# Kernel tuning notes

Measured on AMD Instinct MI355X. Metric: run time of the kernel, lower is better.

Reference implementation:

```python
import jax, jax.numpy as jnp
import numpy as np

T_STEPS = 100
T_EMB = 16
EPS = 1e-8


def sin_emb(t, dim):
    # sinusoidal_time_embedding: [cos(t*f), sin(t*f)] with f = exp(-log(1e4)*i/half)
    half = dim // 2
    freqs = jnp.exp(-jnp.log(jnp.float32(10000.0)) * jnp.arange(half, dtype=jnp.float32) / half)
    a = t.astype(jnp.float32)[:, None] * freqs[None, :]
    return jnp.concatenate([jnp.cos(a), jnp.sin(a)], axis=-1)


def lstm_layer(x_tbf, W_ih, W_hh, b):
    # x_tbf: [T, B, F]; torch gate order i, f, g, o
    B = x_tbf.shape[1]
    H = W_hh.shape[1]

    def step(carry, x_t):
        h, c = carry
        g = x_t @ W_ih.T + h @ W_hh.T + b
        i, f, gg, o = jnp.split(g, 4, axis=-1)
        c = jax.nn.sigmoid(f) * c + jax.nn.sigmoid(i) * jnp.tanh(gg)
        h = jax.nn.sigmoid(o) * jnp.tanh(c)
        return (h, c), h

    z = jnp.zeros((B, H), x_tbf.dtype)
    (h, c), ys = jax.lax.scan(step, (z, z), x_tbf)
    return ys, h


def _forward(x_hist, x_future, y0, turb_idx, pred_steps, init_noise, turb_emb,
             W_ih0, W_hh0, b_ih0, b_hh0, W_ih1, W_hh1, b_ih1, b_hh1,
             W1, b1, W2, b2, W3, b3):
    betas = jnp.linspace(1e-4, 0.02, T_STEPS).astype(jnp.float32)
    alphas = 1.0 - betas
    alpha_bars = jnp.cumprod(alphas)

    B = x_hist.shape[0]
    emb = turb_emb[turb_idx]  # [B, E]
    eh = jnp.broadcast_to(emb[:, None, :], (B, x_hist.shape[1], emb.shape[1]))
    ef = jnp.broadcast_to(emb[:, None, :], (B, x_future.shape[1], emb.shape[1]))
    xh = jnp.concatenate([x_hist, eh], axis=-1).transpose(1, 0, 2)    # [T_in, B, F+E]
    xf = jnp.concatenate([x_future, ef], axis=-1).transpose(1, 0, 2)  # [P, B, exo+E]

    ys0, _ = lstm_layer(xh, W_ih0, W_hh0, b_ih0 + b_hh0)
    _, enc_out = lstm_layer(ys0, W_ih1, W_hh1, b_ih1 + b_hh1)         # [B, H] = h[-1]

    def mlp(x):
        h = jax.nn.relu(x @ W1.T + b1)
        h = jax.nn.relu(h @ W2.T + b2)
        return h @ W3.T + b3

    def ar_step(prev_y, xs):
        exo_t, step, y_init = xs
        cond = jnp.concatenate([enc_out, exo_t, prev_y], axis=1)  # [B, cond_dim]
        h_e = sin_emb(jnp.full((B,), step), T_EMB)

        def dstep(y, t):
            t_e = sin_emb(jnp.full((B,), t), T_EMB)
            eps_hat = mlp(jnp.concatenate([cond, y, t_e, h_e], axis=1))  # [B,1]
            b_t, a_t, ab_t = betas[t], alphas[t], alpha_bars[t]
            pred_x0 = (y - jnp.sqrt(1.0 - ab_t) * eps_hat) / (jnp.sqrt(ab_t) + EPS)
            mean = (y - b_t / (jnp.sqrt(1.0 - ab_t) + EPS) * eps_hat) / (jnp.sqrt(a_t) + EPS)
            # eval mode -> deterministic sampling: posterior noise term is zero
            return jnp.where(t == 0, pred_x0, mean), None

        y, _ = jax.lax.scan(dstep, y_init, jnp.arange(T_STEPS - 1, -1, -1))
        return y, y[:, 0]

    _, seq = jax.lax.scan(ar_step, y0, (xf, jnp.arange(pred_steps), init_noise))
    return seq.T[:, :, None]  # [B, pred_steps, 1]


def setup_inputs() -> dict:
    key = jax.random.key(0)
    ks = list(jax.random.split(key, 24))
    kit = iter(ks)
    B, T_IN, F_IN, EXO, EMB, PRED, HID, NTURB = 1024, 96, 8, 6, 16, 8, 128, 100
    in0 = F_IN + EMB                 # 24
    cond_dim = HID + EXO + EMB + 1   # 151
    in_mlp = cond_dim + 1 + T_EMB + T_EMB  # 184

    def nrm(shape, s=0.05):
        return jax.random.normal(next(kit), shape, jnp.float32) * s

    return {
        'x_hist': jax.random.normal(next(kit), (B, T_IN, F_IN), jnp.float32),
        'x_future': jax.random.normal(next(kit), (B, PRED, EXO), jnp.float32),
        'y0': jnp.zeros((B, 1), jnp.float32),
        'turb_idx': jax.random.randint(next(kit), (B,), 0, NTURB),
        'pred_steps': PRED,
        'init_noise': jax.random.normal(next(kit), (PRED, B, 1), jnp.float32),
        'turb_emb': nrm((NTURB, EMB), 0.1),
        'W_ih0': nrm((4 * HID, in0)), 'W_hh0': nrm((4 * HID, HID)),
        'b_ih0': jnp.zeros((4 * HID,), jnp.float32), 'b_hh0': jnp.zeros((4 * HID,), jnp.float32),
        'W_ih1': nrm((4 * HID, HID)), 'W_hh1': nrm((4 * HID, HID)),
        'b_ih1': jnp.zeros((4 * HID,), jnp.float32), 'b_hh1': jnp.zeros((4 * HID,), jnp.float32),
        'W1': nrm((HID, in_mlp)), 'b1': jnp.zeros((HID,), jnp.float32),
        'W2': nrm((HID, HID)), 'b2': jnp.zeros((HID,), jnp.float32),
        'W3': nrm((1, HID)), 'b3': jnp.zeros((1,), jnp.float32),
    }


def reference(x_hist, x_future, y0, turb_idx, pred_steps, init_noise, turb_emb,
              W_ih0, W_hh0, b_ih0, b_hh0, W_ih1, W_hh1, b_ih1, b_hh1,
              W1, b1, W2, b2, W3, b3):
    return _forward(x_hist, x_future, y0, turb_idx, pred_steps, init_noise, turb_emb,
                    W_ih0, W_hh0, b_ih0, b_hh0, W_ih1, W_hh1, b_ih1, b_hh1,
                    W1, b1, W2, b2, W3, b3)
```

## Files before the change

### kernel.cpp

```cpp
#include <hip/hip_runtime.h>
#include <hip/hip_fp16.h>
#include <stdint.h>


typedef __attribute__((ext_vector_type(2))) _Float16 half2_t;
typedef __attribute__((ext_vector_type(8))) _Float16 v8h;
typedef __attribute__((ext_vector_type(4))) float v4f;

#define DEV __device__ __forceinline__

DEV uint32_t pack2f(float a, float b) {
  __half ha = __float2half_rn(a), hb = __float2half_rn(b);
  return (uint32_t)__half_as_ushort(ha) | ((uint32_t)__half_as_ushort(hb) << 16);
}

DEV float2 up2(uint32_t u) {
  half2_t h = __builtin_bit_cast(half2_t, u);
  return make_float2((float)h.x, (float)h.y);
}

DEV float fast_ex2(float x) {
#if __has_builtin(__builtin_amdgcn_exp2f)
  return __builtin_amdgcn_exp2f(x);
#else
  return exp2f(x);
#endif
}
DEV float fast_rcp(float x) {
#if __has_builtin(__builtin_amdgcn_rcpf)
  return __builtin_amdgcn_rcpf(x);
#else
  return 1.f / x;
#endif
}
DEV float sigm(float x) { return fast_rcp(1.f + fast_ex2(-1.4426950408889634f * x)); }
DEV float tanh_f(float x) {
  return 2.f * fast_rcp(1.f + fast_ex2(-2.8853900817779268f * x)) - 1.f;
}

DEV uint32_t pk_add(uint32_t a, uint32_t b) {
  return __builtin_bit_cast(uint32_t,
      __builtin_bit_cast(half2_t, a) + __builtin_bit_cast(half2_t, b));
}

DEV uint32_t pk_relufma(uint32_t w, uint32_t y, uint32_t b) {
  half2_t r = __builtin_bit_cast(half2_t, w) * __builtin_bit_cast(half2_t, y) +
              __builtin_bit_cast(half2_t, b);
  half2_t z = {(_Float16)0.f, (_Float16)0.f};
#if __has_builtin(__builtin_elementwise_max)
  r = __builtin_elementwise_max(r, z);
#else
  uint32_t u = __builtin_bit_cast(uint32_t, r);
  uint32_t mask = ((u >> 15) & 1u) * 0xFFFFu | ((u >> 31) & 1u) * 0xFFFF0000u;
  r = __builtin_bit_cast(half2_t, u & ~mask);
#endif
  return __builtin_bit_cast(uint32_t, r);
}

DEV uint32_t pk_max0(uint32_t a) {
  half2_t z = {(_Float16)0.f, (_Float16)0.f};
#if __has_builtin(__builtin_elementwise_max)
  return __builtin_bit_cast(uint32_t,
      __builtin_elementwise_max(__builtin_bit_cast(half2_t, a), z));
#else
  uint32_t mask = ((a >> 15) & 1u) * 0xFFFFu | ((a >> 31) & 1u) * 0xFFFF0000u;
  return a & ~mask;
#endif
}

DEV uint32_t cvtpk(float y) {
#if __has_builtin(__builtin_amdgcn_cvt_pkrtz)
  return __builtin_bit_cast(uint32_t, __builtin_amdgcn_cvt_pkrtz(y, y));
#else
  return pack2f(y, y);
#endif
}

DEV uint32_t cvtpk2(float a, float b) {
#if __has_builtin(__builtin_amdgcn_cvt_pkrtz)
  return __builtin_bit_cast(uint32_t, __builtin_amdgcn_cvt_pkrtz(a, b));
#else
  return pack2f(a, b);
#endif
}

DEV half2_t pk_fma2(uint32_t a, uint32_t b, half2_t c) {
  return __builtin_bit_cast(half2_t, a) * __builtin_bit_cast(half2_t, b) + c;
}

static constexpr size_t OFF_XH  = 0;
static constexpr size_t OFF_W0  = 4718592;
static constexpr size_t OFF_BS0 = 4882432;
static constexpr size_t OFF_W1L = 4884480;
static constexpr size_t OFF_BS1 = 5146624;
static constexpr size_t OFF_W2P = 5148672;
static constexpr size_t OFF_ENC = 5181440;
static constexpr size_t OFF_YS0 = 5705728;
static constexpr size_t OFF_TPJ = 30871552;
static constexpr size_t OFF_HPJ = 30897152;
static constexpr size_t OFF_CC  = 30899200;

__global__ void k_prep_xh(const float* __restrict__ xh, const int* __restrict__ tix,
                          const float* __restrict__ temb, uint32_t* __restrict__ out) {
  int idx = blockIdx.x * 256 + threadIdx.x;
  if (idx >= 96 * 1024 * 12) return;
  int m = idx % 12;
  int tb = idx / 12;
  int b = tb & 1023, t = tb >> 10;
  int k0 = 2 * m, k1 = k0 + 1;
  float v0 = (k0 < 8) ? xh[(b * 96 + t) * 8 + k0] : temb[tix[b] * 16 + (k0 - 8)];
  float v1 = (k1 < 8) ? xh[(b * 96 + t) * 8 + k1] : temb[tix[b] * 16 + (k1 - 8)];
  out[idx] = pack2f(v0, v1);
}

__global__ void k_prep_w(const float* __restrict__ Wih0, const float* __restrict__ Whh0,
                         const float* __restrict__ bih0, const float* __restrict__ bhh0,
                         const float* __restrict__ Wih1, const float* __restrict__ Whh1,
                         const float* __restrict__ bih1, const float* __restrict__ bhh1,
                         const float* __restrict__ W2, const float* __restrict__ W1,
                         uint32_t* __restrict__ w0p, uint32_t* __restrict__ w1p,
                         uint32_t* __restrict__ w2p, float* __restrict__ bs0,
                         float* __restrict__ bs1, uint32_t* __restrict__ tpj,
                         uint32_t* __restrict__ hpj, float2* __restrict__ ccg) {
  int idx = blockIdx.x * 256 + threadIdx.x;
  if (idx < 40960) {
    int w = idx / 5120;
    int r = idx % 5120;
    int T = r / 1280; r %= 1280;
    int f = r / 256;  r %= 256;
    int l = r >> 2, c = r & 3;
    int m = l & 15, qf = l >> 4;
    int g = (m & 3) * 128 + w * 16 + (m >> 2) * 4 + T;
    int k0 = f * 32 + qf * 8 + 2 * c, k1 = k0 + 1;
    float a = (k0 < 24) ? Wih0[g * 24 + k0] : ((k0 < 152) ? Whh0[g * 128 + k0 - 24] : 0.f);
    float b = (k1 < 24) ? Wih0[g * 24 + k1] : ((k1 < 152) ? Whh0[g * 128 + k1 - 24] : 0.f);
    w0p[idx] = pack2f(a, b);
  } else if (idx < 106496) {
    int i = idx - 40960;
    int w = i / 8192;
    int r = i % 8192;
    int T = r / 2048; r %= 2048;
    int f = r / 256;  r %= 256;
    int l = r >> 2, c = r & 3;
    int m = l & 15, qf = l >> 4;
    int g = (m & 3) * 128 + w * 16 + (m >> 2) * 4 + T;
    int k0 = f * 32 + qf * 8 + 2 * c, k1 = k0 + 1;
    float a = (k0 < 128) ? Wih1[g * 128 + k0] : Whh1[g * 128 + k0 - 128];
    float b = (k1 < 128) ? Wih1[g * 128 + k1] : Whh1[g * 128 + k1 - 128];
    w1p[i] = pack2f(a, b);
  } else if (idx < 114688) {
    int i = idx - 106496;
    w2p[i] = pack2f(W2[2 * i], W2[2 * i + 1]);
  } else if (idx < 115200) {
    int i = idx - 114688;
    bs0[i] = bih0[i] + bhh0[i];
  } else if (idx < 115712) {
    int i = idx - 115200;
    bs1[i] = bih1[i] + bhh1[i];
  } else if (idx < 122112) {
    int i = idx - 115712;
    int t = i / 64;
    int r = i % 64;
    int q = r / 16, pi = r % 16;
    int k0 = (pi >> 2) * 32 + q * 8 + (pi & 3) * 2;
    float te[16];
#pragma unroll
    for (int j = 0; j < 8; j++) {
      float f = expf(-logf(10000.f) * (float)j / 8.f);
      float a = (float)t * f;
      te[j] = cosf(a);
      te[j + 8] = sinf(a);
    }
    float s0 = 0.f, s1 = 0.f;
#pragma unroll
    for (int j = 0; j < 16; j++) {
      s0 += W1[k0 * 184 + 152 + j] * te[j];
      s1 += W1[(k0 + 1) * 184 + 152 + j] * te[j];
    }
    tpj[i] = pack2f((float)__half2float(__float2half_rn(s0)),
                    (float)__half2float(__float2half_rn(s1)));
  } else if (idx < 122624) {
    int i = idx - 122112;
    int s = i / 64;
    int kp = i % 64;
    float te[16];
#pragma unroll
    for (int j = 0; j < 8; j++) {
      float f = expf(-logf(10000.f) * (float)j / 8.f);
      float a = (float)s * f;
      te[j] = cosf(a);
      te[j + 8] = sinf(a);
    }
    float s0 = 0.f, s1 = 0.f;
#pragma unroll
    for (int j = 0; j < 16; j++) {
      s0 += W1[(2 * kp) * 184 + 168 + j] * te[j];
      s1 += W1[(2 * kp + 1) * 184 + 168 + j] * te[j];
    }
    hpj[i] = pack2f((float)__half2float(__float2half_rn(s0)),
                    (float)__half2float(__float2half_rn(s1)));
  } else if (idx < 122724) {
    int qq = idx - 122624;
    float ab = 1.f, beta = 0.f;
    for (int i = 0; i <= qq; i++) {
      beta = 1e-4f + (0.02f - 1e-4f) * (float)i / 99.f;
      ab *= (1.f - beta);
    }
    float cs, cd;
    if (qq == 0) { cs = sqrtf(1.f - ab); cd = 1.f / (sqrtf(ab) + 1e-8f); }
    else { cs = beta / (sqrtf(1.f - ab) + 1e-8f); cd = 1.f / (sqrtf(1.f - beta) + 1e-8f); }
    ccg[qq] = make_float2(cs * cd, cd);
  }
}

__global__ __launch_bounds__(512, 2) void k_lstm0(const uint32_t* __restrict__ xh16,
                                                  const uint32_t* __restrict__ w0A,
                                                  const float* __restrict__ bs0,
                                                  __half* __restrict__ ys0) {
  __shared__ __align__(16) __half inb[2][16][160];
  const int tid = threadIdx.x;
  const int w = tid >> 6, l = tid & 63;
  const int n = l & 15, ql = l >> 4;
  const int ju = w * 16 + ql * 4;
  const int bbase = blockIdx.x * 16;

  uint4 Af[4][5];
#pragma unroll
  for (int T = 0; T < 4; T++)
#pragma unroll
    for (int f = 0; f < 5; f++)
      Af[T][f] = ((const uint4*)w0A)[((w * 4 + T) * 5 + f) * 64 + l];
  float bias[4][4];
#pragma unroll
  for (int T = 0; T < 4; T++)
#pragma unroll
    for (int r = 0; r < 4; r++) bias[T][r] = bs0[r * 128 + ju + T];

  for (int i = tid; i < 2560; i += 512) ((uint32_t*)inb)[i] = 0u;
  __syncthreads();
  if (tid < 192) {
    int b = tid / 12, m = tid % 12;
    ((uint32_t*)&inb[0][b][0])[m] = xh16[(0 * 1024 + bbase + b) * 12 + m];
  }
  float cst[4] = {0.f, 0.f, 0.f, 0.f};
  __syncthreads();

  for (int t = 0; t < 96; t++) {
    const int cur = t & 1, nxt = cur ^ 1;
    uint32_t sx = 0;
    int sb = 0, sm = 0;
    if (t < 95 && tid < 192) {
      sb = tid / 12; sm = tid % 12;
      sx = xh16[((t + 1) * 1024 + bbase + sb) * 12 + sm];
    }
    v4f acc[4];
#pragma unroll
    for (int T = 0; T < 4; T++) acc[T] = (v4f){0.f, 0.f, 0.f, 0.f};
#pragma unroll
    for (int f = 0; f < 5; f++) {
      uint4 bu = *(const uint4*)&inb[cur][n][f * 32 + ql * 8];
      v8h Bv = __builtin_bit_cast(v8h, bu);
#pragma unroll
      for (int T = 0; T < 4; T++)
        acc[T] = __builtin_amdgcn_mfma_f32_16x16x32_f16(
            __builtin_bit_cast(v8h, Af[T][f]), Bv, acc[T], 0, 0, 0);
    }
    float hv[4];
#pragma unroll
    for (int T = 0; T < 4; T++) {
      float gi = acc[T][0] + bias[T][0];
      float gf = acc[T][1] + bias[T][1];
      float gg = acc[T][2] + bias[T][2];
      float go = acc[T][3] + bias[T][3];
      float c = sigm(gf) * cst[T] + sigm(gi) * tanh_f(gg);
      cst[T] = c;
      hv[T] = sigm(go) * tanh_f(c);
    }
    uint32_t h01 = pack2f(hv[0], hv[1]), h23 = pack2f(hv[2], hv[3]);
    *(uint2*)&inb[nxt][n][24 + ju] = make_uint2(h01, h23);
    *(uint2*)((__half*)ys0 + (size_t)(t * 1024 + bbase + n) * 128 + ju) = make_uint2(h01, h23);
    if (t < 95 && tid < 192) ((uint32_t*)&inb[nxt][sb][0])[sm] = sx;
    __syncthreads();
  }
}

__global__ __launch_bounds__(512, 2) void k_lstm1(const uint32_t* __restrict__ ys0u,
                                                  const uint32_t* __restrict__ w1A,
                                                  const float* __restrict__ bs1,
                                                  float* __restrict__ enc) {
  __shared__ __align__(16) __half inb[2][16][264];
  const int tid = threadIdx.x;
  const int w = tid >> 6, l = tid & 63;
  const int n = l & 15, ql = l >> 4;
  const int ju = w * 16 + ql * 4;
  const int bbase = blockIdx.x * 16;
  const int sb = tid >> 5, sc = tid & 31;

  uint4 Af[4][8];
#pragma unroll
  for (int T = 0; T < 4; T++)
#pragma unroll
    for (int f = 0; f < 8; f++)
      Af[T][f] = ((const uint4*)w1A)[((w * 4 + T) * 8 + f) * 64 + l];
  float bias[4][4];
#pragma unroll
  for (int T = 0; T < 4; T++)
#pragma unroll
    for (int r = 0; r < 4; r++) bias[T][r] = bs1[r * 128 + ju + T];

  for (int i = tid; i < 4224; i += 512) ((uint32_t*)inb)[i] = 0u;
  __syncthreads();
  {
    uint2 v = ((const uint2*)ys0u)[(size_t)(0 * 1024 + bbase + sb) * 32 + sc];
    *(uint2*)&inb[0][sb][sc * 4] = v;
  }
  float cst[4] = {0.f, 0.f, 0.f, 0.f};
  __syncthreads();

  for (int t = 0; t < 96; t++) {
    const int cur = t & 1, nxt = cur ^ 1;
    uint2 sv = make_uint2(0u, 0u);
    if (t < 95)
      sv = ((const uint2*)ys0u)[(size_t)((t + 1) * 1024 + bbase + sb) * 32 + sc];
    v4f acc[4];
#pragma unroll
    for (int T = 0; T < 4; T++) acc[T] = (v4f){0.f, 0.f, 0.f, 0.f};
#pragma unroll
    for (int f = 0; f < 8; f++) {
      uint4 bu = *(const uint4*)&inb[cur][n][f * 32 + ql * 8];
      v8h Bv = __builtin_bit_cast(v8h, bu);
#pragma unroll
      for (int T = 0; T < 4; T++)
        acc[T] = __builtin_amdgcn_mfma_f32_16x16x32_f16(
            __builtin_bit_cast(v8h, Af[T][f]), Bv, acc[T], 0, 0, 0);
    }
    float hv[4];
#pragma unroll
    for (int T = 0; T < 4; T++) {
      float gi = acc[T][0] + bias[T][0];
      float gf = acc[T][1] + bias[T][1];
      float gg = acc[T][2] + bias[T][2];
      float go = acc[T][3] + bias[T][3];
      float c = sigm(gf) * cst[T] + sigm(gi) * tanh_f(gg);
      cst[T] = c;
      hv[T] = sigm(go) * tanh_f(c);
    }
    *(uint2*)&inb[nxt][n][128 + ju] = make_uint2(pack2f(hv[0], hv[1]), pack2f(hv[2], hv[3]));
    if (t < 95) *(uint2*)&inb[nxt][sb][sc * 4] = sv;
    if (t == 95)
      *(float4*)&enc[(size_t)(bbase + n) * 128 + ju] = make_float4(hv[0], hv[1], hv[2], hv[3]);
    __syncthreads();
  }
}

__global__ __launch_bounds__(256, 1) void k_diff(
    const float* __restrict__ xfut, const float* __restrict__ y0,
    const int* __restrict__ tix, const float* __restrict__ noise,
    const float* __restrict__ temb, const float* __restrict__ W1,
    const float* __restrict__ b1, const float* __restrict__ b2,
    const float* __restrict__ W3, const float* __restrict__ b3,
    const uint32_t* __restrict__ w2p, const float* __restrict__ enc,
    const uint32_t* __restrict__ tpj, const uint32_t* __restrict__ hpj,
    const float2* __restrict__ ccG, float* __restrict__ out) {
  __shared__ uint32_t W1sL[128 * 65];
  __shared__ uint32_t W1xL[128 * 29];
  __shared__ uint32_t encPL[16 * 65];
  __shared__ uint32_t embPL[16 * 9];
  __shared__ uint32_t encdL[256 * 17];
  __shared__ __align__(16) float partL[2][16][20];

  const int tid = threadIdx.x;
  const int w = tid >> 6, l = tid & 63;
  const int m = l & 15, q = l >> 4;
  const int gbase = blockIdx.x * 16;
  const uint4* tpj4 = (const uint4*)tpj;

  for (int i = tid; i < 128 * 64; i += 256) {
    int r = i >> 6, c = i & 63;
    W1sL[r * 65 + c] = pack2f(W1[r * 184 + 2 * c], W1[r * 184 + 2 * c + 1]);
  }
  for (int i = tid; i < 128 * 28; i += 256) {
    int r = i / 28, c = i % 28;
    W1xL[r * 29 + c] = pack2f(W1[r * 184 + 128 + 2 * c], W1[r * 184 + 129 + 2 * c]);
  }
  for (int i = tid; i < 16 * 64; i += 256) {
    int bq = i >> 6, c = i & 63;
    encPL[bq * 65 + c] = pack2f(enc[(gbase + bq) * 128 + 2 * c],
                                enc[(gbase + bq) * 128 + 2 * c + 1]);
  }
  for (int i = tid; i < 16 * 8; i += 256) {
    int bq = i >> 3, c = i & 7;
    const float* er = temb + tix[gbase + bq] * 16;
    embPL[bq * 9 + c] = pack2f(er[2 * c], er[2 * c + 1]);
  }
  __syncthreads();

  for (int pi = 0; pi < 16; pi++) {
    int k0 = (pi >> 2) * 32 + q * 8 + (pi & 3) * 2;
    half2_t a0 = {(_Float16)0.f, (_Float16)0.f};
    half2_t a1 = a0;
    const uint32_t* wr0 = &W1sL[k0 * 65];
    const uint32_t* wr1 = &W1sL[(k0 + 1) * 65];
    const uint32_t* ep = &encPL[m * 65];
#pragma unroll 8
    for (int c = 0; c < 64; c++) {
      half2_t e = __builtin_bit_cast(half2_t, ep[c]);
      a0 += __builtin_bit_cast(half2_t, wr0[c]) * e;
      a1 += __builtin_bit_cast(half2_t, wr1[c]) * e;
    }
#pragma unroll
    for (int c = 0; c < 8; c++) {
      half2_t e = __builtin_bit_cast(half2_t, embPL[m * 9 + c]);
      a0 += __builtin_bit_cast(half2_t, W1xL[k0 * 29 + 3 + c]) * e;
      a1 += __builtin_bit_cast(half2_t, W1xL[(k0 + 1) * 29 + 3 + c]) * e;
    }
    float e0 = b1[k0] + (float)a0.x + (float)a0.y;
    float e1 = b1[k0 + 1] + (float)a1.x + (float)a1.y;
    encdL[tid * 17 + pi] = pack2f(e0, e1);
  }

  uint4 Bf[2][4];
  {
    const uint4* w2u4 = (const uint4*)w2p;
#pragma unroll
    for (int j = 0; j < 2; j++)
#pragma unroll
      for (int f = 0; f < 4; f++)
        Bf[j][f] = w2u4[((2 * w + j) * 16 + m) * 16 + f * 4 + q];
  }
  uint32_t b2P[4], w3P[4];
#pragma unroll
  for (int j = 0; j < 2; j++) {
    int tt = 2 * w + j;
    b2P[2 * j]     = pack2f(b2[tt * 16 + q * 4 + 0], b2[tt * 16 + q * 4 + 1]);
    b2P[2 * j + 1] = pack2f(b2[tt * 16 + q * 4 + 2], b2[tt * 16 + q * 4 + 3]);
    w3P[2 * j]     = pack2f(W3[tt * 16 + q * 4 + 0], W3[tt * 16 + q * 4 + 1]);
    w3P[2 * j + 1] = pack2f(W3[tt * 16 + q * 4 + 2], W3[tt * 16 + q * 4 + 3]);
  }
  const float b3v = b3[0];
  const int pslot = w * 4 + q;

  uint32_t w1yP[16];
#pragma unroll
  for (int pi = 0; pi < 16; pi++) {
    int k0 = (pi >> 2) * 32 + q * 8 + (pi & 3) * 2;
    uint32_t ua = W1xL[k0 * 29 + 11];
    uint32_t ub = W1xL[(k0 + 1) * 29 + 11];
    w1yP[pi] = (ua >> 16) | (ub & 0xFFFF0000u);
  }

  float prev_y = y0[gbase + m];
  __syncthreads();

  float y = 0.f;
  float2 ccv = make_float2(0.f, 0.f);
  uint32_t bph[16], bt[16];
  const v4f zf = (v4f){0.f, 0.f, 0.f, 0.f};

#define DSTEP(t_, PB)                                                          \
  do {                                                                         \
    const int tn_ = ((t_) > 0) ? (t_) - 1 : 0;                                 \
    const uint4* tg_ = tpj4 + (size_t)(tn_ * 4 + q) * 4;    \
    uint4 t0 = tg_[0], t1 = tg_[1], t2 = tg_[2], t3 = tg_[3];                  \
    float2 cck_ = ccG[tn_];                                                    \
    const uint32_t yP = cvtpk(y);                                              \
    uint4 au[4];                                                               \
    _Pragma("unroll")                                                          \
    for (int f = 0; f < 4; f++) {                                              \
      au[f].x = pk_relufma(w1yP[4 * f + 0], yP, bt[4 * f + 0]);                \
      au[f].y = pk_relufma(w1yP[4 * f + 1], yP, bt[4 * f + 1]);                \
      au[f].z = pk_relufma(w1yP[4 * f + 2], yP, bt[4 * f + 2]);                \
      au[f].w = pk_relufma(w1yP[4 * f + 3], yP, bt[4 * f + 3]);                \
    }                                                                          \
                             \
    v4f a0 = __builtin_amdgcn_mfma_f32_16x16x32_f16(                           \
        __builtin_bit_cast(v8h, Bf[0][0]), __builtin_bit_cast(v8h, au[0]), zf, 0, 0, 0); \
    v4f b0 = __builtin_amdgcn_mfma_f32_16x16x32_f16(                           \
        __builtin_bit_cast(v8h, Bf[0][1]), __builtin_bit_cast(v8h, au[1]), zf, 0, 0, 0); \
    v4f a1 = __builtin_amdgcn_mfma_f32_16x16x32_f16(                           \
        __builtin_bit_cast(v8h, Bf[1][0]), __builtin_bit_cast(v8h, au[0]), zf, 0, 0, 0); \
    v4f b1x = __builtin_amdgcn_mfma_f32_16x16x32_f16(                          \
        __builtin_bit_cast(v8h, Bf[1][1]), __builtin_bit_cast(v8h, au[1]), zf, 0, 0, 0); \
    a0 = __builtin_amdgcn_mfma_f32_16x16x32_f16(                               \
        __builtin_bit_cast(v8h, Bf[0][2]), __builtin_bit_cast(v8h, au[2]), a0, 0, 0, 0); \
    b0 = __builtin_amdgcn_mfma_f32_16x16x32_f16(                               \
        __builtin_bit_cast(v8h, Bf[0][3]), __builtin_bit_cast(v8h, au[3]), b0, 0, 0, 0); \
    a1 = __builtin_amdgcn_mfma_f32_16x16x32_f16(                               \
        __builtin_bit_cast(v8h, Bf[1][2]), __builtin_bit_cast(v8h, au[2]), a1, 0, 0, 0); \
    b1x = __builtin_amdgcn_mfma_f32_16x16x32_f16(                              \
        __builtin_bit_cast(v8h, Bf[1][3]), __builtin_bit_cast(v8h, au[3]), b1x, 0, 0, 0); \
    v4f c0 = a0 + b0, c1 = a1 + b1x;                                           \
                      \
    half2_t runA = {(_Float16)0.f, (_Float16)0.f};                             \
    half2_t runB = runA;                                                       \
    {                                                                          \
      uint32_t h01 = pk_max0(pk_add(cvtpk2(c0[0], c0[1]), b2P[0]));            \
      uint32_t h23 = pk_max0(pk_add(cvtpk2(c0[2], c0[3]), b2P[1]));            \
      runA = pk_fma2(h01, w3P[0], runA);                                       \
      runA = pk_fma2(h23, w3P[1], runA);                                       \
      uint32_t g01 = pk_max0(pk_add(cvtpk2(c1[0], c1[1]), b2P[2]));            \
      uint32_t g23 = pk_max0(pk_add(cvtpk2(c1[2], c1[3]), b2P[3]));            \
      runB = pk_fma2(g01, w3P[2], runB);                                       \
      runB = pk_fma2(g23, w3P[3], runB);                                       \
    }                                                                          \
    partL[PB][m][pslot] = ((float)runA.x + (float)runA.y) +                    \
                          ((float)runB.x + (float)runB.y);                     \
    const float pre_ = ccv.y * y - ccv.x * b3v;           \
    __syncthreads();                                                           \
               \
    const v4f* pl_ = (const v4f*)&partL[PB][m][0];                             \
    v4f p0_ = pl_[0], p1_ = pl_[1], p2_ = pl_[2], p3_ = pl_[3];                \
    bt[0] = pk_add(bph[0], t0.x);   bt[1] = pk_add(bph[1], t0.y);              \
    bt[2] = pk_add(bph[2], t0.z);   bt[3] = pk_add(bph[3], t0.w);              \
    bt[4] = pk_add(bph[4], t1.x);   bt[5] = pk_add(bph[5], t1.y);              \
    bt[6] = pk_add(bph[6], t1.z);   bt[7] = pk_add(bph[7], t1.w);              \
    bt[8] = pk_add(bph[8], t2.x);   bt[9] = pk_add(bph[9], t2.y);              \
    bt[10] = pk_add(bph[10], t2.z); bt[11] = pk_add(bph[11], t2.w);            \
    bt[12] = pk_add(bph[12], t3.x); bt[13] = pk_add(bph[13], t3.y);            \
    bt[14] = pk_add(bph[14], t3.z); bt[15] = pk_add(bph[15], t3.w);            \
    v4f ps_ = (p0_ + p1_) + (p2_ + p3_);                                       \
    y = pre_ - ccv.x * ((ps_[0] + ps_[1]) + (ps_[2] + ps_[3]));                \
    ccv = cck_;                                                                \
  } while (0)

  for (int s = 0; s < 8; s++) {
    float yn = noise[s * 1024 + gbase + m];
    float xf[6];
#pragma unroll
    for (int i = 0; i < 6; i++) xf[i] = xfut[((gbase + m) * 8 + s) * 6 + i];
#pragma unroll
    for (int pi = 0; pi < 16; pi++) {
      int k0 = (pi >> 2) * 32 + q * 8 + (pi & 3) * 2;
      float2 ed = up2(encdL[tid * 17 + pi]);
      float e0 = ed.x, e1 = ed.y;
#pragma unroll
      for (int c = 0; c < 3; c++) {
        float2 w0v = up2(W1xL[k0 * 29 + c]);
        float2 w1v = up2(W1xL[(k0 + 1) * 29 + c]);
        e0 += w0v.x * xf[2 * c] + w0v.y * xf[2 * c + 1];
        e1 += w1v.x * xf[2 * c] + w1v.y * xf[2 * c + 1];
      }
      e0 += up2(W1xL[k0 * 29 + 11]).x * prev_y;
      e1 += up2(W1xL[(k0 + 1) * 29 + 11]).x * prev_y;
      float2 hh = up2(hpj[s * 64 + (k0 >> 1)]);
      e0 += hh.x;
      e1 += hh.y;
      bph[pi] = pack2f(e0, e1);
    }

    y = yn;
    {
      const uint4* tg = tpj4 + (size_t)(99 * 4 + q) * 4;
      uint4 t0 = tg[0], t1 = tg[1], t2 = tg[2], t3 = tg[3];
      bt[0] = pk_add(bph[0], t0.x);   bt[1] = pk_add(bph[1], t0.y);
      bt[2] = pk_add(bph[2], t0.z);   bt[3] = pk_add(bph[3], t0.w);
      bt[4] = pk_add(bph[4], t1.x);   bt[5] = pk_add(bph[5], t1.y);
      bt[6] = pk_add(bph[6], t1.z);   bt[7] = pk_add(bph[7], t1.w);
      bt[8] = pk_add(bph[8], t2.x);   bt[9] = pk_add(bph[9], t2.y);
      bt[10] = pk_add(bph[10], t2.z); bt[11] = pk_add(bph[11], t2.w);
      bt[12] = pk_add(bph[12], t3.x); bt[13] = pk_add(bph[13], t3.y);
      bt[14] = pk_add(bph[14], t3.z); bt[15] = pk_add(bph[15], t3.w);
    }
    ccv = ccG[99];

    for (int it = 0; it < 50; it++) {
      DSTEP(99 - 2 * it, 0);
      DSTEP(98 - 2 * it, 1);
    }

    if (w == 0 && l < 16) out[(gbase + l) * 8 + s] = y;
    prev_y = y;
  }
#undef DSTEP
}

extern "C" void kernel_launch(void* const* d_in, const int* in_sizes, int n_in,
                              void* d_out, int out_size, void* d_ws, size_t ws_size,
                              hipStream_t stream) {
  const float* x_hist    = (const float*)d_in[0];
  const float* x_future  = (const float*)d_in[1];
  const float* y0        = (const float*)d_in[2];
  const int*   turb_idx  = (const int*)d_in[3];
  const float* init_noise = (const float*)d_in[5];
  const float* turb_emb  = (const float*)d_in[6];
  const float* W_ih0     = (const float*)d_in[7];
  const float* W_hh0     = (const float*)d_in[8];
  const float* b_ih0     = (const float*)d_in[9];
  const float* b_hh0     = (const float*)d_in[10];
  const float* W_ih1     = (const float*)d_in[11];
  const float* W_hh1     = (const float*)d_in[12];
  const float* b_ih1     = (const float*)d_in[13];
  const float* b_hh1     = (const float*)d_in[14];
  const float* W1        = (const float*)d_in[15];
  const float* b1        = (const float*)d_in[16];
  const float* W2        = (const float*)d_in[17];
  const float* b2        = (const float*)d_in[18];
  const float* W3        = (const float*)d_in[19];
  const float* b3        = (const float*)d_in[20];

  char* ws = (char*)d_ws;
  uint32_t* xh16 = (uint32_t*)(ws + OFF_XH);
  uint32_t* w0p  = (uint32_t*)(ws + OFF_W0);
  float*    bs0  = (float*)(ws + OFF_BS0);
  uint32_t* w1p  = (uint32_t*)(ws + OFF_W1L);
  float*    bs1  = (float*)(ws + OFF_BS1);
  uint32_t* w2p  = (uint32_t*)(ws + OFF_W2P);
  float*    encf = (float*)(ws + OFF_ENC);
  __half*   ys0h = (__half*)(ws + OFF_YS0);
  uint32_t* tpjw = (uint32_t*)(ws + OFF_TPJ);
  uint32_t* hpjw = (uint32_t*)(ws + OFF_HPJ);
  float2*   ccw  = (float2*)(ws + OFF_CC);

  k_prep_xh<<<4608, 256, 0, stream>>>(x_hist, turb_idx, turb_emb, xh16);
  k_prep_w<<<480, 256, 0, stream>>>(W_ih0, W_hh0, b_ih0, b_hh0,
                                    W_ih1, W_hh1, b_ih1, b_hh1,
                                    W2, W1, w0p, w1p, w2p, bs0, bs1,
                                    tpjw, hpjw, ccw);
  k_lstm0<<<64, 512, 0, stream>>>(xh16, w0p, bs0, ys0h);
  k_lstm1<<<64, 512, 0, stream>>>((const uint32_t*)ys0h, w1p, bs1, encf);
  k_diff<<<64, 256, 0, stream>>>(x_future, y0, turb_idx, init_noise, turb_emb,
                                 W1, b1, b2, W3, b3, w2p, encf,
                                 tpjw, hpjw, ccw, (float*)d_out);
}
```

Baseline: 633.2 us.

## Interleave two independent batch chains per diffusion block to halve barriers

The diffusion kernel now processes 32 batch rows per block as two independent 16-row chains (A and B), so 32 blocks launch instead of 64. Each denoising step computes both chains before one shared barrier, giving the scheduler independent MFMA and ALU work to interleave and spreading the per-step sync cost over twice the rows. In exchange, fewer CUs are used, register pressure roughly doubles for the bias arrays, and shared-memory use grows.

```diff
diff --git a/kernel.cpp b/kernel.cpp
--- a/kernel.cpp
+++ b/kernel.cpp
@@ -364,15 +364,15 @@
     const float2* __restrict__ ccG, float* __restrict__ out) {
   __shared__ uint32_t W1sL[128 * 65];
   __shared__ uint32_t W1xL[128 * 29];
-  __shared__ uint32_t encPL[16 * 65];
-  __shared__ uint32_t embPL[16 * 9];
-  __shared__ uint32_t encdL[256 * 17];
-  __shared__ __align__(16) float partL[2][16][20];
+  __shared__ uint32_t encPL[32 * 65];
+  __shared__ uint32_t embPL[32 * 9];
+  __shared__ uint32_t encdL[2][256 * 17];
+  __shared__ __align__(16) float partL[2][2][16][20];
 
   const int tid = threadIdx.x;
   const int w = tid >> 6, l = tid & 63;
   const int m = l & 15, q = l >> 4;
-  const int gbase = blockIdx.x * 16;
+  const int gbase = blockIdx.x * 32;
   const uint4* tpj4 = (const uint4*)tpj;
 
   for (int i = tid; i < 128 * 64; i += 256) {
@@ -383,40 +383,44 @@
     int r = i / 28, c = i % 28;
     W1xL[r * 29 + c] = pack2f(W1[r * 184 + 128 + 2 * c], W1[r * 184 + 129 + 2 * c]);
   }
-  for (int i = tid; i < 16 * 64; i += 256) {
+  for (int i = tid; i < 32 * 64; i += 256) {
     int bq = i >> 6, c = i & 63;
     encPL[bq * 65 + c] = pack2f(enc[(gbase + bq) * 128 + 2 * c],
                                 enc[(gbase + bq) * 128 + 2 * c + 1]);
   }
-  for (int i = tid; i < 16 * 8; i += 256) {
+  for (int i = tid; i < 32 * 8; i += 256) {
     int bq = i >> 3, c = i & 7;
     const float* er = temb + tix[gbase + bq] * 16;
     embPL[bq * 9 + c] = pack2f(er[2 * c], er[2 * c + 1]);
   }
   __syncthreads();
 
-  for (int pi = 0; pi < 16; pi++) {
-    int k0 = (pi >> 2) * 32 + q * 8 + (pi & 3) * 2;
-    half2_t a0 = {(_Float16)0.f, (_Float16)0.f};
-    half2_t a1 = a0;
-    const uint32_t* wr0 = &W1sL[k0 * 65];
-    const uint32_t* wr1 = &W1sL[(k0 + 1) * 65];
-    const uint32_t* ep = &encPL[m * 65];
+#pragma unroll
+  for (int ch = 0; ch < 2; ch++) {
+    const int bm = ch * 16 + m;
+    for (int pi = 0; pi < 16; pi++) {
+      int k0 = (pi >> 2) * 32 + q * 8 + (pi & 3) * 2;
+      half2_t a0 = {(_Float16)0.f, (_Float16)0.f};
+      half2_t a1 = a0;
+      const uint32_t* wr0 = &W1sL[k0 * 65];
+      const uint32_t* wr1 = &W1sL[(k0 + 1) * 65];
+      const uint32_t* ep = &encPL[bm * 65];
 #pragma unroll 8
-    for (int c = 0; c < 64; c++) {
-      half2_t e = __builtin_bit_cast(half2_t, ep[c]);
-      a0 += __builtin_bit_cast(half2_t, wr0[c]) * e;
-      a1 += __builtin_bit_cast(half2_t, wr1[c]) * e;
-    }
-#pragma unroll
-    for (int c = 0; c < 8; c++) {
-      half2_t e = __builtin_bit_cast(half2_t, embPL[m * 9 + c]);
-      a0 += __builtin_bit_cast(half2_t, W1xL[k0 * 29 + 3 + c]) * e;
-      a1 += __builtin_bit_cast(half2_t, W1xL[(k0 + 1) * 29 + 3 + c]) * e;
-    }
-    float e0 = b1[k0] + (float)a0.x + (float)a0.y;
-    float e1 = b1[k0 + 1] + (float)a1.x + (float)a1.y;
-    encdL[tid * 17 + pi] = pack2f(e0, e1);
+      for (int c = 0; c < 64; c++) {
+        half2_t e = __builtin_bit_cast(half2_t, ep[c]);
+        a0 += __builtin_bit_cast(half2_t, wr0[c]) * e;
+        a1 += __builtin_bit_cast(half2_t, wr1[c]) * e;
+      }
+#pragma unroll
+      for (int c = 0; c < 8; c++) {
+        half2_t e = __builtin_bit_cast(half2_t, embPL[bm * 9 + c]);
+        a0 += __builtin_bit_cast(half2_t, W1xL[k0 * 29 + 3 + c]) * e;
+        a1 += __builtin_bit_cast(half2_t, W1xL[(k0 + 1) * 29 + 3 + c]) * e;
+      }
+      float e0 = b1[k0] + (float)a0.x + (float)a0.y;
+      float e1 = b1[k0 + 1] + (float)a1.x + (float)a1.y;
+      encdL[ch][tid * 17 + pi] = pack2f(e0, e1);
+    }
   }
 
   uint4 Bf[2][4];
@@ -449,30 +453,26 @@
     w1yP[pi] = (ua >> 16) | (ub & 0xFFFF0000u);
   }
 
-  float prev_y = y0[gbase + m];
+  float prevA = y0[gbase + m];
+  float prevB = y0[gbase + 16 + m];
   __syncthreads();
 
-  float y = 0.f;
+  float yA = 0.f, yB = 0.f;
   float2 ccv = make_float2(0.f, 0.f);
-  uint32_t bph[16], bt[16];
+  uint32_t bphA[16], btA[16], bphB[16], btB[16];
   const v4f zf = (v4f){0.f, 0.f, 0.f, 0.f};
 
-#define DSTEP(t_, PB)                                                          \
+#define CHAIN_COMPUTE(Y, BT, CH, PB)                                           \
   do {                                                                         \
-    const int tn_ = ((t_) > 0) ? (t_) - 1 : 0;                                 \
-    const uint4* tg_ = tpj4 + (size_t)(tn_ * 4 + q) * 4;    \
-    uint4 t0 = tg_[0], t1 = tg_[1], t2 = tg_[2], t3 = tg_[3];                  \
-    float2 cck_ = ccG[tn_];                                                    \
-    const uint32_t yP = cvtpk(y);                                              \
+    const uint32_t yP = cvtpk(Y);                                              \
     uint4 au[4];                                                               \
     _Pragma("unroll")                                                          \
     for (int f = 0; f < 4; f++) {                                              \
-      au[f].x = pk_relufma(w1yP[4 * f + 0], yP, bt[4 * f + 0]);                \
-      au[f].y = pk_relufma(w1yP[4 * f + 1], yP, bt[4 * f + 1]);                \
-      au[f].z = pk_relufma(w1yP[4 * f + 2], yP, bt[4 * f + 2]);                \
-      au[f].w = pk_relufma(w1yP[4 * f + 3], yP, bt[4 * f + 3]);                \
+      au[f].x = pk_relufma(w1yP[4 * f + 0], yP, BT[4 * f + 0]);                \
+      au[f].y = pk_relufma(w1yP[4 * f + 1], yP, BT[4 * f + 1]);                \
+      au[f].z = pk_relufma(w1yP[4 * f + 2], yP, BT[4 * f + 2]);                \
+      au[f].w = pk_relufma(w1yP[4 * f + 3], yP, BT[4 * f + 3]);                \
     }                                                                          \
-                             \
     v4f a0 = __builtin_amdgcn_mfma_f32_16x16x32_f16(                           \
         __builtin_bit_cast(v8h, Bf[0][0]), __builtin_bit_cast(v8h, au[0]), zf, 0, 0, 0); \
     v4f b0 = __builtin_amdgcn_mfma_f32_16x16x32_f16(                           \
@@ -490,7 +490,6 @@
     b1x = __builtin_amdgcn_mfma_f32_16x16x32_f16(                              \
         __builtin_bit_cast(v8h, Bf[1][3]), __builtin_bit_cast(v8h, au[3]), b1x, 0, 0, 0); \
     v4f c0 = a0 + b0, c1 = a1 + b1x;                                           \
-                      \
     half2_t runA = {(_Float16)0.f, (_Float16)0.f};                             \
     half2_t runB = runA;                                                       \
     {                                                                          \
@@ -503,63 +502,103 @@
       runB = pk_fma2(g01, w3P[2], runB);                                       \
       runB = pk_fma2(g23, w3P[3], runB);                                       \
     }                                                                          \
-    partL[PB][m][pslot] = ((float)runA.x + (float)runA.y) +                    \
-                          ((float)runB.x + (float)runB.y);                     \
-    const float pre_ = ccv.y * y - ccv.x * b3v;           \
+    partL[PB][CH][m][pslot] = ((float)runA.x + (float)runA.y) +                \
+                              ((float)runB.x + (float)runB.y);                 \
+  } while (0)
+
+#define DSTEP(t_, PB)                                                          \
+  do {                                                                         \
+    const int tn_ = ((t_) > 0) ? (t_) - 1 : 0;                                 \
+    const uint4* tg_ = tpj4 + (size_t)(tn_ * 4 + q) * 4;           \
+    uint4 t0 = tg_[0], t1 = tg_[1], t2 = tg_[2], t3 = tg_[3];                  \
+    float2 cck_ = ccG[tn_];                                                    \
+    CHAIN_COMPUTE(yA, btA, 0, PB);                                             \
+    CHAIN_COMPUTE(yB, btB, 1, PB);                                             \
+    const float preA_ = ccv.y * yA - ccv.x * b3v;                              \
+    const float preB_ = ccv.y * yB - ccv.x * b3v;                              \
     __syncthreads();                                                           \
-               \
-    const v4f* pl_ = (const v4f*)&partL[PB][m][0];                             \
-    v4f p0_ = pl_[0], p1_ = pl_[1], p2_ = pl_[2], p3_ = pl_[3];                \
-    bt[0] = pk_add(bph[0], t0.x);   bt[1] = pk_add(bph[1], t0.y);              \
-    bt[2] = pk_add(bph[2], t0.z);   bt[3] = pk_add(bph[3], t0.w);              \
-    bt[4] = pk_add(bph[4], t1.x);   bt[5] = pk_add(bph[5], t1.y);              \
-    bt[6] = pk_add(bph[6], t1.z);   bt[7] = pk_add(bph[7], t1.w);              \
-    bt[8] = pk_add(bph[8], t2.x);   bt[9] = pk_add(bph[9], t2.y);              \
-    bt[10] = pk_add(bph[10], t2.z); bt[11] = pk_add(bph[11], t2.w);            \
-    bt[12] = pk_add(bph[12], t3.x); bt[13] = pk_add(bph[13], t3.y);            \
-    bt[14] = pk_add(bph[14], t3.z); bt[15] = pk_add(bph[15], t3.w);            \
-    v4f ps_ = (p0_ + p1_) + (p2_ + p3_);                                       \
-    y = pre_ - ccv.x * ((ps_[0] + ps_[1]) + (ps_[2] + ps_[3]));                \
+    const v4f* plA_ = (const v4f*)&partL[PB][0][m][0];                         \
+    v4f pA0_ = plA_[0], pA1_ = plA_[1], pA2_ = plA_[2], pA3_ = plA_[3];        \
+    const v4f* plB_ = (const v4f*)&partL[PB][1][m][0];                         \
+    v4f pB0_ = plB_[0], pB1_ = plB_[1], pB2_ = plB_[2], pB3_ = plB_[3];        \
+    btA[0] = pk_add(bphA[0], t0.x);   btA[1] = pk_add(bphA[1], t0.y);          \
+    btA[2] = pk_add(bphA[2], t0.z);   btA[3] = pk_add(bphA[3], t0.w);          \
+    btA[4] = pk_add(bphA[4], t1.x);   btA[5] = pk_add(bphA[5], t1.y);          \
+    btA[6] = pk_add(bphA[6], t1.z);   btA[7] = pk_add(bphA[7], t1.w);          \
+    btA[8] = pk_add(bphA[8], t2.x);   btA[9] = pk_add(bphA[9], t2.y);          \
+    btA[10] = pk_add(bphA[10], t2.z); btA[11] = pk_add(bphA[11], t2.w);        \
+    btA[12] = pk_add(bphA[12], t3.x); btA[13] = pk_add(bphA[13], t3.y);        \
+    btA[14] = pk_add(bphA[14], t3.z); btA[15] = pk_add(bphA[15], t3.w);        \
+    btB[0] = pk_add(bphB[0], t0.x);   btB[1] = pk_add(bphB[1], t0.y);          \
+    btB[2] = pk_add(bphB[2], t0.z);   btB[3] = pk_add(bphB[3], t0.w);          \
+    btB[4] = pk_add(bphB[4], t1.x);   btB[5] = pk_add(bphB[5], t1.y);          \
+    btB[6] = pk_add(bphB[6], t1.z);   btB[7] = pk_add(bphB[7], t1.w);          \
+    btB[8] = pk_add(bphB[8], t2.x);   btB[9] = pk_add(bphB[9], t2.y);          \
+    btB[10] = pk_add(bphB[10], t2.z); btB[11] = pk_add(bphB[11], t2.w);        \
+    btB[12] = pk_add(bphB[12], t3.x); btB[13] = pk_add(bphB[13], t3.y);        \
+    btB[14] = pk_add(bphB[14], t3.z); btB[15] = pk_add(bphB[15], t3.w);        \
+    v4f psA_ = (pA0_ + pA1_) + (pA2_ + pA3_);                                  \
+    v4f psB_ = (pB0_ + pB1_) + (pB2_ + pB3_);                                  \
+    yA = preA_ - ccv.x * ((psA_[0] + psA_[1]) + (psA_[2] + psA_[3]));          \
+    yB = preB_ - ccv.x * ((psB_[0] + psB_[1]) + (psB_[2] + psB_[3]));          \
     ccv = cck_;                                                                \
   } while (0)
 
   for (int s = 0; s < 8; s++) {
-    float yn = noise[s * 1024 + gbase + m];
-    float xf[6];
-#pragma unroll
-    for (int i = 0; i < 6; i++) xf[i] = xfut[((gbase + m) * 8 + s) * 6 + i];
+    float ynA = noise[s * 1024 + gbase + m];
+    float ynB = noise[s * 1024 + gbase + 16 + m];
+    float xfA[6], xfB[6];
+#pragma unroll
+    for (int i = 0; i < 6; i++) {
+      xfA[i] = xfut[((gbase + m) * 8 + s) * 6 + i];
+      xfB[i] = xfut[((gbase + 16 + m) * 8 + s) * 6 + i];
+    }
 #pragma unroll
     for (int pi = 0; pi < 16; pi++) {
       int k0 = (pi >> 2) * 32 + q * 8 + (pi & 3) * 2;
-      float2 ed = up2(encdL[tid * 17 + pi]);
-      float e0 = ed.x, e1 = ed.y;
+      float2 hh = up2(hpj[s * 64 + (k0 >> 1)]);
+      float2 edA = up2(encdL[0][tid * 17 + pi]);
+      float2 edB = up2(encdL[1][tid * 17 + pi]);
+      float eA0 = edA.x + hh.x, eA1 = edA.y + hh.y;
+      float eB0 = edB.x + hh.x, eB1 = edB.y + hh.y;
 #pragma unroll
       for (int c = 0; c < 3; c++) {
         float2 w0v = up2(W1xL[k0 * 29 + c]);
         float2 w1v = up2(W1xL[(k0 + 1) * 29 + c]);
-        e0 += w0v.x * xf[2 * c] + w0v.y * xf[2 * c + 1];
-        e1 += w1v.x * xf[2 * c] + w1v.y * xf[2 * c + 1];
+        eA0 += w0v.x * xfA[2 * c] + w0v.y * xfA[2 * c + 1];
+        eA1 += w1v.x * xfA[2 * c] + w1v.y * xfA[2 * c + 1];
+        eB0 += w0v.x * xfB[2 * c] + w0v.y * xfB[2 * c + 1];
+        eB1 += w1v.x * xfB[2 * c] + w1v.y * xfB[2 * c + 1];
       }
-      e0 += up2(W1xL[k0 * 29 + 11]).x * prev_y;
-      e1 += up2(W1xL[(k0 + 1) * 29 + 11]).x * prev_y;
-      float2 hh = up2(hpj[s * 64 + (k0 >> 1)]);
-      e0 += hh.x;
-      e1 += hh.y;
-      bph[pi] = pack2f(e0, e1);
-    }
-
-    y = yn;
+      float wy0 = up2(W1xL[k0 * 29 + 11]).x;
+      float wy1 = up2(W1xL[(k0 + 1) * 29 + 11]).x;
+      eA0 += wy0 * prevA;  eA1 += wy1 * prevA;
+      eB0 += wy0 * prevB;  eB1 += wy1 * prevB;
+      bphA[pi] = pack2f(eA0, eA1);
+      bphB[pi] = pack2f(eB0, eB1);
+    }
+
+    yA = ynA;
+    yB = ynB;
     {
       const uint4* tg = tpj4 + (size_t)(99 * 4 + q) * 4;
       uint4 t0 = tg[0], t1 = tg[1], t2 = tg[2], t3 = tg[3];
-      bt[0] = pk_add(bph[0], t0.x);   bt[1] = pk_add(bph[1], t0.y);
-      bt[2] = pk_add(bph[2], t0.z);   bt[3] = pk_add(bph[3], t0.w);
-      bt[4] = pk_add(bph[4], t1.x);   bt[5] = pk_add(bph[5], t1.y);
-      bt[6] = pk_add(bph[6], t1.z);   bt[7] = pk_add(bph[7], t1.w);
-      bt[8] = pk_add(bph[8], t2.x);   bt[9] = pk_add(bph[9], t2.y);
-      bt[10] = pk_add(bph[10], t2.z); bt[11] = pk_add(bph[11], t2.w);
-      bt[12] = pk_add(bph[12], t3.x); bt[13] = pk_add(bph[13], t3.y);
-      bt[14] = pk_add(bph[14], t3.z); bt[15] = pk_add(bph[15], t3.w);
+      btA[0] = pk_add(bphA[0], t0.x);   btA[1] = pk_add(bphA[1], t0.y);
+      btA[2] = pk_add(bphA[2], t0.z);   btA[3] = pk_add(bphA[3], t0.w);
+      btA[4] = pk_add(bphA[4], t1.x);   btA[5] = pk_add(bphA[5], t1.y);
+      btA[6] = pk_add(bphA[6], t1.z);   btA[7] = pk_add(bphA[7], t1.w);
+      btA[8] = pk_add(bphA[8], t2.x);   btA[9] = pk_add(bphA[9], t2.y);
+      btA[10] = pk_add(bphA[10], t2.z); btA[11] = pk_add(bphA[11], t2.w);
+      btA[12] = pk_add(bphA[12], t3.x); btA[13] = pk_add(bphA[13], t3.y);
+      btA[14] = pk_add(bphA[14], t3.z); btA[15] = pk_add(bphA[15], t3.w);
+      btB[0] = pk_add(bphB[0], t0.x);   btB[1] = pk_add(bphB[1], t0.y);
+      btB[2] = pk_add(bphB[2], t0.z);   btB[3] = pk_add(bphB[3], t0.w);
+      btB[4] = pk_add(bphB[4], t1.x);   btB[5] = pk_add(bphB[5], t1.y);
+      btB[6] = pk_add(bphB[6], t1.z);   btB[7] = pk_add(bphB[7], t1.w);
+      btB[8] = pk_add(bphB[8], t2.x);   btB[9] = pk_add(bphB[9], t2.y);
+      btB[10] = pk_add(bphB[10], t2.z); btB[11] = pk_add(bphB[11], t2.w);
+      btB[12] = pk_add(bphB[12], t3.x); btB[13] = pk_add(bphB[13], t3.y);
+      btB[14] = pk_add(bphB[14], t3.z); btB[15] = pk_add(bphB[15], t3.w);
     }
     ccv = ccG[99];
 
@@ -568,10 +607,13 @@
       DSTEP(98 - 2 * it, 1);
     }
 
-    if (w == 0 && l < 16) out[(gbase + l) * 8 + s] = y;
-    prev_y = y;
+    if (w == 0 && l < 16) out[(gbase + l) * 8 + s] = yA;
+    if (w == 1 && l < 16) out[(gbase + 16 + l) * 8 + s] = yB;
+    prevA = yA;
+    prevB = yB;
   }
 #undef DSTEP
+#undef CHAIN_COMPUTE
 }
 
 extern "C" void kernel_launch(void* const* d_in, const int* in_sizes, int n_in,
@@ -618,7 +660,7 @@
                                     tpjw, hpjw, ccw);
   k_lstm0<<<64, 512, 0, stream>>>(xh16, w0p, bs0, ys0h);
   k_lstm1<<<64, 512, 0, stream>>>((const uint32_t*)ys0h, w1p, bs1, encf);
-  k_diff<<<64, 256, 0, stream>>>(x_future, y0, turb_idx, init_noise, turb_emb,
+  k_diff<<<32, 256, 0, stream>>>(x_future, y0, turb_idx, init_noise, turb_emb,
                                  W1, b1, b2, W3, b3, w2p, encf,
                                  tpjw, hpjw, ccw, (float*)d_out);
 }
```

New measurement: 857.2 us. +35.4%, slower.
